# Kernel optimization log

Hardware: AMD Instinct MI355X
Metric: run time of the kernel (lower is better)

Reference implementation:

```python
import jax, jax.numpy as jnp
import numpy as np

NEG_SLOPE = 0.2  # PyG GATConv default leaky_relu slope


def gat_conv(h_in, src, dst, W, a_src, a_dst, b, N):
    # h_in: [N, Fin]; src/dst: [E] (self-loops already appended)
    h = h_in @ W                      # [N, Fout]
    alpha_src = h @ a_src             # [N]
    alpha_dst = h @ a_dst             # [N]
    e = jax.nn.leaky_relu(alpha_src[src] + alpha_dst[dst], NEG_SLOPE)  # [E]
    # segment softmax over incoming edges of each destination node
    m = jax.ops.segment_max(e, dst, num_segments=N)
    m = jnp.where(jnp.isfinite(m), m, 0.0)
    p = jnp.exp(e - m[dst])
    denom = jax.ops.segment_sum(p, dst, num_segments=N)
    alpha = p / jnp.maximum(denom[dst], 1e-16)
    out = jax.ops.segment_sum(alpha[:, None] * h[src], dst, num_segments=N)
    return out + b


def setup_inputs() -> dict:
    key = jax.random.key(0)
    ks = jax.random.split(key, 16)
    N, E, V, D, H, C, G = 100000, 1600000, 128, 50, 16, 10, 512
    x = jax.random.normal(ks[0], (N, V), dtype=jnp.float32)
    edge_index = jax.random.randint(ks[1], (2, E), 0, N, dtype=jnp.int32)
    batch = jnp.sort(jax.random.randint(ks[2], (N,), 0, G, dtype=jnp.int32))
    s = lambda fan: 1.0 / np.sqrt(fan)
    return {
        "x": x, "edge_index": edge_index, "batch": batch,
        "embedding": jax.random.normal(ks[3], (V, D), dtype=jnp.float32),
        "W1": jax.random.normal(ks[4], (D, H), dtype=jnp.float32) * s(D),
        "a_src1": jax.random.normal(ks[5], (H,), dtype=jnp.float32) * s(H),
        "a_dst1": jax.random.normal(ks[6], (H,), dtype=jnp.float32) * s(H),
        "b1": jnp.zeros((H,), dtype=jnp.float32),
        "W2": jax.random.normal(ks[7], (H, H), dtype=jnp.float32) * s(H),
        "a_src2": jax.random.normal(ks[8], (H,), dtype=jnp.float32) * s(H),
        "a_dst2": jax.random.normal(ks[9], (H,), dtype=jnp.float32) * s(H),
        "b2": jnp.zeros((H,), dtype=jnp.float32),
        "W3": jax.random.normal(ks[10], (H, C), dtype=jnp.float32) * s(H),
        "a_src3": jax.random.normal(ks[11], (C,), dtype=jnp.float32) * s(C),
        "a_dst3": jax.random.normal(ks[12], (C,), dtype=jnp.float32) * s(C),
        "b3": jnp.zeros((C,), dtype=jnp.float32),
    }


def reference(x, edge_index, batch, embedding, W1, a_src1, a_dst1, b1,
              W2, a_src2, a_dst2, b2, W3, a_src3, a_dst3, b3):
    N = x.shape[0]
    G = 512  # num graphs
    # embedding lookup via argmax over one-hot-ish features
    idx = jnp.argmax(x, axis=1)
    h = embedding[idx]                               # [N, 50]
    # add self-loops once (PyG GATConv default)
    loops = jnp.arange(N, dtype=edge_index.dtype)
    src = jnp.concatenate([edge_index[0], loops])
    dst = jnp.concatenate([edge_index[1], loops])
    h = jax.nn.relu(gat_conv(h, src, dst, W1, a_src1, a_dst1, b1, N))
    # dropout: eval mode -> identity
    h = jax.nn.relu(gat_conv(h, src, dst, W2, a_src2, a_dst2, b2, N))
    h = gat_conv(h, src, dst, W3, a_src3, a_dst3, b3, N)  # [N, C]
    # global mean pool over graphs
    sums = jax.ops.segment_sum(h, batch, num_segments=G)
    cnts = jax.ops.segment_sum(jnp.ones((N,), h.dtype), batch, num_segments=G)
    pooled = sums / jnp.maximum(cnts, 1.0)[:, None]
    return jax.nn.softmax(pooled, axis=1)
```

## Files before the change

### kernel.cpp

```cpp
#include <hip/hip_runtime.h>
#include <math.h>

#define NEG_SLOPE 0.2f
#define NBUK_MAX 2048

typedef float v4f __attribute__((ext_vector_type(4)));

template <int B2>
__global__ void __launch_bounds__(1024)
k_histarg(const float* __restrict__ x, const int* __restrict__ edst, int E,
          int* __restrict__ histT, int NBUK, int* __restrict__ idx, int N, int V) {
    __shared__ int sh[NBUK_MAX];
    int t = threadIdx.x;
    if ((int)blockIdx.x < B2) {
        int b = blockIdx.x;
        for (int k = t; k < NBUK; k += 1024) sh[k] = 0;
        __syncthreads();
        long long ebeg = (long long)b * E / B2, eend = (long long)(b + 1) * E / B2;
        for (long long i = ebeg + t; i < eend; i += 1024)
            atomicAdd(&sh[__builtin_nontemporal_load(edst + i) >> 6], 1);
        __syncthreads();
        for (int k = t; k < NBUK; k += 1024) histT[(long long)k * B2 + b] = sh[k];
    } else {
        int node = ((int)blockIdx.x - B2) * 32 + (t >> 5);
        int lane = t & 31;
        if (node >= N) return;
        const v4f* row = (const v4f*)(x + (long long)node * V);
        float bv = -INFINITY;
        int bi = 0x7fffffff;
        int nq = V >> 2;
        for (int q = lane; q < nq; q += 32) {
            v4f v = __builtin_nontemporal_load(row + q);
            int base = q << 2;
            if (v.x > bv || (v.x == bv && base     < bi)) { bv = v.x; bi = base;     }
            if (v.y > bv || (v.y == bv && base + 1 < bi)) { bv = v.y; bi = base + 1; }
            if (v.z > bv || (v.z == bv && base + 2 < bi)) { bv = v.z; bi = base + 2; }
            if (v.w > bv || (v.w == bv && base + 3 < bi)) { bv = v.w; bi = base + 3; }
        }
        for (int off = 16; off > 0; off >>= 1) {
            float ov = __shfl_down(bv, off, 32);
            int   oi = __shfl_down(bi, off, 32);
            if (ov > bv || (ov == bv && oi < bi)) { bv = ov; bi = oi; }
        }
        if (lane == 0) idx[node] = bi;
    }
}

template <int FIN, int FOUT>
__global__ void __launch_bounds__(256)
k_scan_tr(const int* __restrict__ vals, int* __restrict__ excl, int* __restrict__ bsums, int M,
          const float* __restrict__ emb, const int* __restrict__ idx,
          const float* __restrict__ W, const float* __restrict__ a_src,
          const float* __restrict__ a_dst, _Float16* __restrict__ h_t,
          float* __restrict__ asrc, float* __restrict__ adst, int N, int NB_SCAN) {
    __shared__ int s[256];
    __shared__ float sW[FIN * FOUT];
    __shared__ float sa[FOUT], sd[FOUT];
    int t = threadIdx.x;
    if ((int)blockIdx.x < NB_SCAN) {
        int i = blockIdx.x * 256 + t;
        int v = (i < M) ? vals[i] : 0;
        s[t] = v;
        __syncthreads();
        for (int off = 1; off < 256; off <<= 1) {
            int a = (t >= off) ? s[t - off] : 0;
            __syncthreads();
            s[t] += a;
            __syncthreads();
        }
        if (i < M) excl[i] = s[t] - v;
        if (t == 255) bsums[blockIdx.x] = s[255];
    } else {
        for (int i = t; i < FIN * FOUT; i += 256) sW[i] = W[i];
        if (t < FOUT) { sa[t] = a_src[t]; sd[t] = a_dst[t]; }
        __syncthreads();
        int n = ((int)blockIdx.x - NB_SCAN) * 256 + t;
        if (n >= N) return;
        float acc[FOUT];
#pragma unroll
        for (int f = 0; f < FOUT; f++) acc[f] = 0.f;
        const float* hr = emb + (long long)idx[n] * FIN;
        for (int k = 0; k < FIN; k++) {
            float v = hr[k];
#pragma unroll
            for (int f = 0; f < FOUT; f++) acc[f] += v * sW[k * FOUT + f];
        }
        float s1 = 0.f, s2 = 0.f;
        _Float16 hh[16];
#pragma unroll
        for (int f = 0; f < 16; f++) hh[f] = (_Float16)0.f;
#pragma unroll
        for (int f = 0; f < FOUT; f++) {
            hh[f] = (_Float16)acc[f];
            s1 += acc[f] * sa[f];
            s2 += acc[f] * sd[f];
        }
        uint4* dst = (uint4*)(h_t + (long long)n * 16);
        dst[0] = ((uint4*)hh)[0];
        dst[1] = ((uint4*)hh)[1];
        asrc[n] = s1;
        adst[n] = s2;
    }
}

template <int B2>
__global__ void __launch_bounds__(1024)
k_scatB(const int* __restrict__ esrc, const int* __restrict__ edst, int E,
        const int* __restrict__ sexcl, const int* __restrict__ bsums,
        int* __restrict__ tmp, int NBUK) {
    __shared__ int cur[NBUK_MAX];
    __shared__ int pb[NBUK_MAX];
    int t = threadIdx.x, b = blockIdx.x;
    {
        int v0 = (t < NBUK) ? bsums[t] : 0;
        int v1 = (t + 1024 < NBUK) ? bsums[t + 1024] : 0;
        pb[t] = v0;
        pb[t + 1024] = v1;
        __syncthreads();
        for (int off = 1; off < 2048; off <<= 1) {
            int a0 = (t >= off) ? pb[t - off] : 0;
            int a1 = (t + 1024 >= off) ? pb[t + 1024 - off] : 0;
            __syncthreads();
            pb[t] += a0;
            pb[t + 1024] += a1;
            __syncthreads();
        }
        int e0 = pb[t] - v0, e1 = pb[t + 1024] - v1;
        __syncthreads();
        pb[t] = e0;
        pb[t + 1024] = e1;
        __syncthreads();
    }
    for (int k = t; k < NBUK; k += 1024)
        cur[k] = sexcl[(long long)k * B2 + b] + pb[k];
    __syncthreads();
    long long ebeg = (long long)b * E / B2, eend = (long long)(b + 1) * E / B2;
    for (long long i = ebeg + t; i < eend; i += 1024) {
        int d = __builtin_nontemporal_load(edst + i);
        int s = __builtin_nontemporal_load(esrc + i);
        int pos = atomicAdd(&cur[d >> 6], 1);
        __builtin_nontemporal_store(((d & 63) << 18) | s, tmp + pos);
    }
}

template <int B2>
__global__ void __launch_bounds__(256)
k_binB(const int* __restrict__ sexcl, const int* __restrict__ bsums,
       const int* __restrict__ tmp,
       int* __restrict__ rowptr, int* __restrict__ csr_src, int N, int NBUK, int E) {
    __shared__ int cnt[64];
    __shared__ int cur[64];
    __shared__ int red[256];
    int t = threadIdx.x, b = blockIdx.x;
    int part = 0;
    for (int i = t; i < b; i += 256) part += bsums[i];
    red[t] = part;
    __syncthreads();
    for (int str = 128; str > 0; str >>= 1) {
        if (t < str) red[t] += red[t + str];
        __syncthreads();
    }
    int pb_b  = red[0];
    int pb_b1 = pb_b + bsums[b];
    int t0 = sexcl[(long long)b * B2] + pb_b;
    int t1 = (b + 1 < NBUK) ? (sexcl[(long long)(b + 1) * B2] + pb_b1) : E;

    if (t < 64) cnt[t] = 0;
    __syncthreads();
    for (int i = t0 + t; i < t1; i += 256) atomicAdd(&cnt[tmp[i] >> 18], 1);
    __syncthreads();
    if (t < 64) {
        int v = cnt[t];
        int incl = v;
        for (int off = 1; off < 64; off <<= 1) {
            int u = __shfl_up(incl, off, 64);
            if (t >= off) incl += u;
        }
        int base = t0 + incl - v;
        int d = (b << 6) + t;
        if (d < N) rowptr[d] = base;
        cur[t] = base;
        if (d == N - 1) rowptr[N] = E;
    }
    __syncthreads();
    for (int i = t0 + t; i < t1; i += 256) {
        int p = tmp[i];
        int pos = atomicAdd(&cur[p >> 18], 1);
        csr_src[pos] = p & 0x3FFFF;
    }
}

template <typename EPI>
__device__ __forceinline__ void gat_core(const int* __restrict__ rowptr,
                                         const int* __restrict__ csr_src,
                                         const float* __restrict__ asrc,
                                         const float* __restrict__ adst,
                                         const _Float16* __restrict__ h_t,
                                         int N, int grp, int lane, EPI epilogue) {
    int d = grp;
    int r0 = rowptr[d], r1 = rowptr[d + 1];
    float ad = adst[d];

    float e0 = asrc[d] + ad;
    e0 = (e0 >= 0.f) ? e0 : NEG_SLOPE * e0;
    float p0 = __expf(e0);
    float acc  = p0 * (float)h_t[(long long)d * 16 + lane];
    float psum = (lane == 0) ? p0 : 0.f;

    int j = r0;
    if (j < r1) {
        int myj = j + lane;
        bool valid = myj < r1;
        int s = valid ? __builtin_nontemporal_load(csr_src + myj) : d;
        float a = asrc[s];
        while (true) {
            int jn = j + 16;
            int s2 = d; float a2 = 0.f; bool validn = false;
            if (jn < r1) {
                int myjn = jn + lane;
                validn = myjn < r1;
                s2 = validn ? __builtin_nontemporal_load(csr_src + myjn) : d;
                a2 = asrc[s2];
            }
            float e = a + ad;
            e = (e >= 0.f) ? e : NEG_SLOPE * e;
            float p = valid ? __expf(e) : 0.f;
            psum += p;
#pragma unroll
            for (int k = 0; k < 16; k++) {
                float pk = __shfl(p, k, 16);
                int   sk = __shfl(s, k, 16);
                acc += pk * (float)h_t[(long long)sk * 16 + lane];
            }
            if (jn >= r1) break;
            j = jn; s = s2; a = a2; valid = validn;
        }
    }
    for (int off = 8; off > 0; off >>= 1) psum += __shfl_xor(psum, off, 16);
    epilogue(d, acc / fmaxf(psum, 1e-16f));
}

template <int FN>
__global__ void k_gat_ft(const int* __restrict__ rowptr, const int* __restrict__ csr_src,
                         const float* __restrict__ asrc, const float* __restrict__ adst,
                         const _Float16* __restrict__ h_t, const float* __restrict__ bias,
                         const float* __restrict__ Wn, const float* __restrict__ an_src,
                         const float* __restrict__ an_dst,
                         _Float16* __restrict__ h_next, float* __restrict__ asrc_n,
                         float* __restrict__ adst_n, int N) {
    __shared__ float sW[16 * FN];
    __shared__ float sa[FN], sd[FN], sb[16];
    for (int i = threadIdx.x; i < 16 * FN; i += blockDim.x) sW[i] = Wn[i];
    if (threadIdx.x < FN) { sa[threadIdx.x] = an_src[threadIdx.x]; sd[threadIdx.x] = an_dst[threadIdx.x]; }
    if (threadIdx.x < 16) sb[threadIdx.x] = bias[threadIdx.x];
    __syncthreads();

    int grp  = (blockIdx.x * blockDim.x + threadIdx.x) >> 4;
    int lane = threadIdx.x & 15;
    if (grp >= N) return;

    gat_core(rowptr, csr_src, asrc, adst, h_t, N, grp, lane,
        [&](int d, float v) {
            v = fmaxf(v + sb[lane], 0.f);
            float acc2 = 0.f;
#pragma unroll
            for (int k = 0; k < 16; k++) {
                float vk = __shfl(v, k, 16);
                if (lane < FN) acc2 += vk * sW[k * FN + lane];
            }
            float c1 = (lane < FN) ? acc2 * sa[lane] : 0.f;
            float c2 = (lane < FN) ? acc2 * sd[lane] : 0.f;
            for (int off = 8; off > 0; off >>= 1) {
                c1 += __shfl_xor(c1, off, 16);
                c2 += __shfl_xor(c2, off, 16);
            }
            h_next[(long long)d * 16 + lane] = (_Float16)((lane < FN) ? acc2 : 0.f);
            if (lane == 0) { asrc_n[d] = c1; adst_n[d] = c2; }
        });
}

template <int FOUT>
__global__ void k_gat_last(const int* __restrict__ rowptr, const int* __restrict__ csr_src,
                           const float* __restrict__ asrc, const float* __restrict__ adst,
                           const _Float16* __restrict__ h_t, float* __restrict__ out, int N) {
    int grp  = (blockIdx.x * blockDim.x + threadIdx.x) >> 4;
    int lane = threadIdx.x & 15;
    if (grp >= N) return;
    gat_core(rowptr, csr_src, asrc, adst, h_t, N, grp, lane,
        [&](int d, float v) {
            if (lane < FOUT) out[(long long)d * FOUT + lane] = v;
        });
}

__global__ void k_pool(const float* __restrict__ h3, const int* __restrict__ batch,
                       const float* __restrict__ b3, float* __restrict__ out, int N, int C) {
    int g = blockIdx.x;
    int lo = 0, hi = N;
    while (lo < hi) { int mid = (lo + hi) >> 1; if (batch[mid] < g) lo = mid + 1; else hi = mid; }
    int start = lo;
    hi = N;
    while (lo < hi) { int mid = (lo + hi) >> 1; if (batch[mid] < g + 1) lo = mid + 1; else hi = mid; }
    int end = lo;

    float sum[16];
    for (int f = 0; f < C; f++) sum[f] = 0.f;
    for (int n = start + threadIdx.x; n < end; n += blockDim.x) {
        const float* r = h3 + (long long)n * C;
        for (int f = 0; f < C; f++) sum[f] += r[f];
    }
    __shared__ float red[256 * 16];
    for (int f = 0; f < C; f++) red[threadIdx.x * 16 + f] = sum[f];
    __syncthreads();
    for (int str = blockDim.x / 2; str > 0; str >>= 1) {
        if ((int)threadIdx.x < str)
            for (int f = 0; f < C; f++) red[threadIdx.x * 16 + f] += red[(threadIdx.x + str) * 16 + f];
        __syncthreads();
    }
    if (threadIdx.x == 0) {
        float cnt = fmaxf((float)(end - start), 1.f);
        float vals[16];
        float mx = -INFINITY;
        for (int f = 0; f < C; f++) { vals[f] = red[f] / cnt + b3[f]; mx = fmaxf(mx, vals[f]); }
        float se = 0.f;
        for (int f = 0; f < C; f++) { vals[f] = __expf(vals[f] - mx); se += vals[f]; }
        for (int f = 0; f < C; f++) out[(long long)g * C + f] = vals[f] / se;
    }
}

extern "C" void kernel_launch(void* const* d_in, const int* in_sizes, int n_in,
                              void* d_out, int out_size, void* d_ws, size_t ws_size,
                              hipStream_t stream) {
    const float* x    = (const float*)d_in[0];
    const int*   eidx = (const int*)d_in[1];
    const int*   batch= (const int*)d_in[2];
    const float* emb  = (const float*)d_in[3];
    const float* W1   = (const float*)d_in[4];
    const float* as1  = (const float*)d_in[5];
    const float* ad1  = (const float*)d_in[6];
    const float* b1   = (const float*)d_in[7];
    const float* W2   = (const float*)d_in[8];
    const float* as2  = (const float*)d_in[9];
    const float* ad2  = (const float*)d_in[10];
    const float* b2   = (const float*)d_in[11];
    const float* W3   = (const float*)d_in[12];
    const float* as3  = (const float*)d_in[13];
    const float* ad3  = (const float*)d_in[14];
    const float* b3   = (const float*)d_in[15];

    const int H = in_sizes[5];
    const int C = in_sizes[13];
    const int D = in_sizes[4] / H;
    const int V = in_sizes[3] / D;
    const int N = in_sizes[0] / V;
    const int E = in_sizes[1] / 2;
    const int G = out_size / C;
    const int* esrc = eidx;
    const int* edst = eidx + E;
    const int NBUK = (N + 63) >> 6;
    constexpr int B2 = 256;
    const int M = NBUK * B2;

    char* w = (char*)d_ws;
    auto carve = [&](size_t bytes) {
        char* p = w;
        w += (bytes + 255) & ~(size_t)255;
        return p;
    };
    float*     as_a    = (float*)carve((size_t)N * 4);
    float*     ad_a    = (float*)carve((size_t)N * 4);
    float*     as_b    = (float*)carve((size_t)N * 4);
    float*     ad_b    = (float*)carve((size_t)N * 4);
    int*       idx     = (int*)carve((size_t)N * 4);
    int*       rowptr  = (int*)carve((size_t)(N + 1) * 4);
    int*       csr_src = (int*)carve((size_t)E * 4);
    int*       histT   = (int*)carve((size_t)M * 4);
    int*       sexcl   = (int*)carve((size_t)M * 4);
    int*       bsums   = (int*)carve(2048 * 4);
    _Float16*  hTa     = (_Float16*)carve((size_t)N * 16 * 2);
    _Float16*  hTb     = (_Float16*)carve((size_t)N * 16 * 2);
    size_t zone_bytes = ((size_t)E * 4 > (size_t)N * C * 4) ? (size_t)E * 4 : (size_t)N * C * 4;
    char*  zone = carve(zone_bytes);
    float* X0  = (float*)zone;
    int*   tmp = (int*)zone;
    (void)ws_size; (void)n_in;

    const int BT = 256;
    dim3 blk(BT);
    int gGat  = (N * 16 + BT - 1) / BT;
    int nb2   = (M + 255) / 256;
    int gArg  = (N + 31) / 32;
    int gTr   = (N + BT - 1) / BT;

    k_histarg<B2><<<B2 + gArg, dim3(1024), 0, stream>>>(x, edst, E, histT, NBUK, idx, N, V);

    k_scan_tr<50, 16><<<nb2 + gTr, blk, 0, stream>>>(histT, sexcl, bsums, M,
                                                     emb, idx, W1, as1, ad1, hTa, as_a, ad_a, N, nb2);

    k_scatB<B2><<<B2, dim3(1024), 0, stream>>>(esrc, edst, E, sexcl, bsums, tmp, NBUK);
    k_binB<B2><<<NBUK, blk, 0, stream>>>(sexcl, bsums, tmp, rowptr, csr_src, N, NBUK, E);

    k_gat_ft<16><<<gGat, blk, 0, stream>>>(rowptr, csr_src, as_a, ad_a, hTa, b1,
                                           W2, as2, ad2, hTb, as_b, ad_b, N);

    k_gat_ft<10><<<gGat, blk, 0, stream>>>(rowptr, csr_src, as_b, ad_b, hTb, b2,
                                           W3, as3, ad3, hTa, as_a, ad_a, N);

    k_gat_last<10><<<gGat, blk, 0, stream>>>(rowptr, csr_src, as_a, ad_a, hTa, X0, N);

    k_pool<<<G, blk, 0, stream>>>(X0, batch, b3, (float*)d_out, N, C);
}
```

Measured before the change: 301.5 us.

## Hoist block-sum scan into separate kernel and drop nontemporal memory hints

Adds a single-block scan kernel that turns the block sums into exclusive prefixes once, in place. Previously every scatter block re-ran a 2048-entry shared-memory scan and every bin block re-reduced all earlier block sums. All nontemporal loads and stores become ordinary accesses so the edge and CSR data can stay in cache. The cost is an extra serial kernel launch, and the rewrite assumes NBUK equals nb2 for bsums indexing.

```diff
diff --git a/kernel.cpp b/kernel.cpp
--- a/kernel.cpp
+++ b/kernel.cpp
@@ -18,7 +18,7 @@
         __syncthreads();
         long long ebeg = (long long)b * E / B2, eend = (long long)(b + 1) * E / B2;
         for (long long i = ebeg + t; i < eend; i += 1024)
-            atomicAdd(&sh[__builtin_nontemporal_load(edst + i) >> 6], 1);
+            atomicAdd(&sh[edst[i] >> 6], 1);
         __syncthreads();
         for (int k = t; k < NBUK; k += 1024) histT[(long long)k * B2 + b] = sh[k];
     } else {
@@ -30,7 +30,7 @@
         int bi = 0x7fffffff;
         int nq = V >> 2;
         for (int q = lane; q < nq; q += 32) {
-            v4f v = __builtin_nontemporal_load(row + q);
+            v4f v = row[q];
             int base = q << 2;
             if (v.x > bv || (v.x == bv && base     < bi)) { bv = v.x; bi = base;     }
             if (v.y > bv || (v.y == bv && base + 1 < bi)) { bv = v.y; bi = base + 1; }
@@ -103,43 +103,41 @@
     }
 }
 
+__global__ void k_scan2(int* __restrict__ bsums, int nb) {
+    __shared__ int s[2048];
+    int i = threadIdx.x;
+    int v0 = (i < nb) ? bsums[i] : 0;
+    int v1 = (i + 1024 < nb) ? bsums[i + 1024] : 0;
+    s[i] = v0;
+    s[i + 1024] = v1;
+    __syncthreads();
+    for (int off = 1; off < 2048; off <<= 1) {
+        int a0 = (i >= off) ? s[i - off] : 0;
+        int a1 = (i + 1024 >= off) ? s[i + 1024 - off] : 0;
+        __syncthreads();
+        s[i] += a0;
+        s[i + 1024] += a1;
+        __syncthreads();
+    }
+    if (i < nb) bsums[i] = s[i] - v0;
+    if (i + 1024 < nb) bsums[i + 1024] = s[i + 1024] - v1;
+}
+
 template <int B2>
 __global__ void __launch_bounds__(1024)
 k_scatB(const int* __restrict__ esrc, const int* __restrict__ edst, int E,
         const int* __restrict__ sexcl, const int* __restrict__ bsums,
         int* __restrict__ tmp, int NBUK) {
     __shared__ int cur[NBUK_MAX];
-    __shared__ int pb[NBUK_MAX];
     int t = threadIdx.x, b = blockIdx.x;
-    {
-        int v0 = (t < NBUK) ? bsums[t] : 0;
-        int v1 = (t + 1024 < NBUK) ? bsums[t + 1024] : 0;
-        pb[t] = v0;
-        pb[t + 1024] = v1;
-        __syncthreads();
-        for (int off = 1; off < 2048; off <<= 1) {
-            int a0 = (t >= off) ? pb[t - off] : 0;
-            int a1 = (t + 1024 >= off) ? pb[t + 1024 - off] : 0;
-            __syncthreads();
-            pb[t] += a0;
-            pb[t + 1024] += a1;
-            __syncthreads();
-        }
-        int e0 = pb[t] - v0, e1 = pb[t + 1024] - v1;
-        __syncthreads();
-        pb[t] = e0;
-        pb[t + 1024] = e1;
-        __syncthreads();
-    }
     for (int k = t; k < NBUK; k += 1024)
-        cur[k] = sexcl[(long long)k * B2 + b] + pb[k];
+        cur[k] = sexcl[(long long)k * B2 + b] + bsums[k];
     __syncthreads();
     long long ebeg = (long long)b * E / B2, eend = (long long)(b + 1) * E / B2;
     for (long long i = ebeg + t; i < eend; i += 1024) {
-        int d = __builtin_nontemporal_load(edst + i);
-        int s = __builtin_nontemporal_load(esrc + i);
+        int d = edst[i];
         int pos = atomicAdd(&cur[d >> 6], 1);
-        __builtin_nontemporal_store(((d & 63) << 18) | s, tmp + pos);
+        tmp[pos] = ((d & 63) << 18) | esrc[i];
     }
 }
 
@@ -150,21 +148,9 @@
        int* __restrict__ rowptr, int* __restrict__ csr_src, int N, int NBUK, int E) {
     __shared__ int cnt[64];
     __shared__ int cur[64];
-    __shared__ int red[256];
     int t = threadIdx.x, b = blockIdx.x;
-    int part = 0;
-    for (int i = t; i < b; i += 256) part += bsums[i];
-    red[t] = part;
-    __syncthreads();
-    for (int str = 128; str > 0; str >>= 1) {
-        if (t < str) red[t] += red[t + str];
-        __syncthreads();
-    }
-    int pb_b  = red[0];
-    int pb_b1 = pb_b + bsums[b];
-    int t0 = sexcl[(long long)b * B2] + pb_b;
-    int t1 = (b + 1 < NBUK) ? (sexcl[(long long)(b + 1) * B2] + pb_b1) : E;
-
+    int t0 = sexcl[(long long)b * B2] + bsums[b];
+    int t1 = (b + 1 < NBUK) ? (sexcl[(long long)(b + 1) * B2] + bsums[b + 1]) : E;
     if (t < 64) cnt[t] = 0;
     __syncthreads();
     for (int i = t0 + t; i < t1; i += 256) atomicAdd(&cnt[tmp[i] >> 18], 1);
@@ -211,7 +197,7 @@
     if (j < r1) {
         int myj = j + lane;
         bool valid = myj < r1;
-        int s = valid ? __builtin_nontemporal_load(csr_src + myj) : d;
+        int s = valid ? csr_src[myj] : d;
         float a = asrc[s];
         while (true) {
             int jn = j + 16;
@@ -219,7 +205,7 @@
             if (jn < r1) {
                 int myjn = jn + lane;
                 validn = myjn < r1;
-                s2 = validn ? __builtin_nontemporal_load(csr_src + myjn) : d;
+                s2 = validn ? csr_src[myjn] : d;
                 a2 = asrc[s2];
             }
             float e = a + ad;
@@ -395,6 +381,7 @@
 
     k_scan_tr<50, 16><<<nb2 + gTr, blk, 0, stream>>>(histT, sexcl, bsums, M,
                                                      emb, idx, W1, as1, ad1, hTa, as_a, ad_a, N, nb2);
+    k_scan2<<<1, 1024, 0, stream>>>(bsums, nb2);
 
     k_scatB<B2><<<B2, dim3(1024), 0, stream>>>(esrc, edst, E, sexcl, bsums, tmp, NBUK);
     k_binB<B2><<<NBUK, blk, 0, stream>>>(sexcl, bsums, tmp, rowptr, csr_src, N, NBUK, E);
```

Result: faster. 268.2 us (-11.1%).
